# Kernel optimization log

Measured on AMD Instinct MI355X. Metric: run time of the kernel, lower is better.

## Reference

```python
import jax, jax.numpy as jnp
import numpy as np

N_NODES = 100000
NEG_SLOPE = 0.01  # torch F.leaky_relu default

def _degrees(edge_src, edge_dst, n):
    ones = jnp.ones(edge_src.shape[0], dtype=jnp.float32)
    dout = jax.ops.segment_sum(ones, edge_src, num_segments=n)
    din = jax.ops.segment_sum(ones, edge_dst, num_segments=n)
    # DGL clamps zero degrees to 1 (norm='both')
    dout_inv_sqrt = jax.lax.rsqrt(jnp.maximum(dout, 1.0))
    din_inv_sqrt = jax.lax.rsqrt(jnp.maximum(din, 1.0))
    return dout_inv_sqrt, din_inv_sqrt

def _graph_conv(x, W, b, edge_src, edge_dst, dout_is, din_is, n):
    # DGL GraphConv, norm='both': h_i = b + sum_{j->i} (x_j W) / sqrt(d_out(j) d_in(i))
    h = (x * dout_is[:, None]) @ W            # [N, out]
    agg = jax.ops.segment_sum(h[edge_src], edge_dst, num_segments=n)
    return agg * din_is[:, None] + b

def setup_inputs() -> dict:
    key = jax.random.key(0)
    ks = jax.random.split(key, 16)
    n, e = N_NODES, 1600000
    features = jax.random.normal(ks[0], (n, 4), dtype=jnp.float32)
    edge_src = jax.random.randint(ks[1], (e,), 0, n, dtype=jnp.int32)
    edge_dst = jax.random.randint(ks[2], (e,), 0, n, dtype=jnp.int32)
    dims = [(4, 128), (128, 128), (128, 128), (128, 128), (128, 3)]
    inp = {"features": features, "edge_src": edge_src, "edge_dst": edge_dst}
    for i, (fi, fo) in enumerate(dims):
        s = (2.0 / (fi + fo)) ** 0.5  # glorot
        inp[f"W{i+1}"] = jax.random.normal(ks[3 + i], (fi, fo), dtype=jnp.float32) * s
        inp[f"b{i+1}"] = jnp.zeros((fo,), dtype=jnp.float32)
    return inp

def reference(features, edge_src, edge_dst, W1, b1, W2, b2, W3, b3, W4, b4, W5, b5):
    n = features.shape[0]
    dout_is, din_is = _degrees(edge_src, edge_dst, n)
    lrelu = lambda x: jnp.where(x >= 0, x, NEG_SLOPE * x)
    x = lrelu(_graph_conv(features, W1, b1, edge_src, edge_dst, dout_is, din_is, n))
    x = lrelu(_graph_conv(x, W2, b2, edge_src, edge_dst, dout_is, din_is, n))
    x = lrelu(_graph_conv(x, W3, b3, edge_src, edge_dst, dout_is, din_is, n))
    x = lrelu(_graph_conv(x, W4, b4, edge_src, edge_dst, dout_is, din_is, n))
    x = _graph_conv(x, W5, b5, edge_src, edge_dst, dout_is, din_is, n)
    return x
```

## Files before the change

### kernel.cpp

```cpp
#include <hip/hip_runtime.h>
#include <hip/hip_fp16.h>
#include <math.h>


#define LRELU_SLOPE 0.01f
#define XPAD 129
#define MAXBUCK 512


__device__ inline void chunk_range(int E, int nchunks, int cid, int& lo, int& hi) {
    int chunk = (E + nchunks - 1) / nchunks;
    lo = cid * chunk;
    hi = min(E, lo + chunk);
}

__global__ __launch_bounds__(256) void k_part_hist2(const int* __restrict__ src, const int* __restrict__ dst,
                                                    int E, int nbuck,
                                                    unsigned* __restrict__ gHistS, unsigned* __restrict__ gHistD,
                                                    unsigned* __restrict__ blockBaseS, unsigned* __restrict__ blockBaseD) {
    __shared__ unsigned hs[MAXBUCK];
    __shared__ unsigned hd[MAXBUCK];
    for (int i = threadIdx.x; i < nbuck; i += 256) { hs[i] = 0u; hd[i] = 0u; }
    __syncthreads();
    int lo, hi;
    chunk_range(E, gridDim.x, blockIdx.x, lo, hi);
    for (int e = lo + threadIdx.x; e < hi; e += 256) {
        atomicAdd(&hs[src[e] >> 8], 1u);
        atomicAdd(&hd[dst[e] >> 8], 1u);
    }
    __syncthreads();
    for (int i = threadIdx.x; i < nbuck; i += 256) {
        blockBaseS[(size_t)blockIdx.x * nbuck + i] = atomicAdd(&gHistS[i], hs[i]);
        blockBaseD[(size_t)blockIdx.x * nbuck + i] = atomicAdd(&gHistD[i], hd[i]);
    }
}

__global__ __launch_bounds__(512) void k_part_scan(const unsigned* __restrict__ gHist, int nbuck,
                                                   unsigned* __restrict__ bucketStart,
                                                   unsigned* __restrict__ row_ptr_last, unsigned Eval) {
    __shared__ unsigned s[MAXBUCK];
    int t = threadIdx.x;
    s[t] = (t < nbuck) ? gHist[t] : 0u;
    __syncthreads();
    for (int off = 1; off < MAXBUCK; off <<= 1) {
        unsigned v = (t >= off) ? s[t - off] : 0u;
        __syncthreads();
        s[t] += v;
        __syncthreads();
    }
    if (t <= nbuck) bucketStart[t] = (t == 0) ? 0u : s[t - 1];
    if (t == 0 && row_ptr_last) *row_ptr_last = Eval;
}

__global__ __launch_bounds__(256) void k_part_scatter_both(const int* __restrict__ src, const int* __restrict__ dst,
                                                           int E, int nbuck,
                                                           const unsigned* __restrict__ bstartS,
                                                           const unsigned* __restrict__ bstartD,
                                                           const unsigned* __restrict__ blockBaseS,
                                                           const unsigned* __restrict__ blockBaseD,
                                                           int2* __restrict__ pairs, int* __restrict__ srcbuf) {
    __shared__ unsigned curS[MAXBUCK];
    __shared__ unsigned curD[MAXBUCK];
    for (int i = threadIdx.x; i < nbuck; i += 256) {
        curS[i] = bstartS[i] + blockBaseS[(size_t)blockIdx.x * nbuck + i];
        curD[i] = bstartD[i] + blockBaseD[(size_t)blockIdx.x * nbuck + i];
    }
    __syncthreads();
    int lo, hi;
    chunk_range(E, gridDim.x, blockIdx.x, lo, hi);
    for (int e = lo + threadIdx.x; e < hi; e += 256) {
        int s = src[e], d = dst[e];
        unsigned posD = atomicAdd(&curD[d >> 8], 1u);
        pairs[posD] = make_int2(s, d);
        unsigned posS = atomicAdd(&curS[s >> 8], 1u);
        srcbuf[posS] = s;
    }
}

__global__ __launch_bounds__(256) void k_bucket_csr(const int2* __restrict__ pairs,
                                                    const unsigned* __restrict__ bucketStart,
                                                    unsigned* __restrict__ row_ptr,
                                                    unsigned* __restrict__ din_cnt,
                                                    int* __restrict__ csr, int n) {
    __shared__ unsigned hist[256];
    __shared__ unsigned scanw[256];
    __shared__ unsigned cur[256];
    int b = blockIdx.x, t = threadIdx.x;
    unsigned beg = bucketStart[b], end = bucketStart[b + 1];
    hist[t] = 0u;
    __syncthreads();
    for (unsigned e = beg + t; e < end; e += 256)
        atomicAdd(&hist[pairs[e].y & 255], 1u);
    __syncthreads();
    scanw[t] = hist[t];
    __syncthreads();
    for (int off = 1; off < 256; off <<= 1) {
        unsigned u = (t >= off) ? scanw[t - off] : 0u;
        __syncthreads();
        scanw[t] += u;
        __syncthreads();
    }
    unsigned excl = scanw[t] - hist[t];
    int node = (b << 8) + t;
    if (node < n) {
        row_ptr[node] = beg + excl;
        din_cnt[node] = hist[t];
    }
    cur[t] = excl;
    __syncthreads();
    for (unsigned e = beg + t; e < end; e += 256) {
        int2 p = pairs[e];
        unsigned pos = beg + atomicAdd(&cur[p.y & 255], 1u);
        csr[pos] = p.x;
    }
}

__global__ __launch_bounds__(256) void k_bucket_cnt(const int* __restrict__ vals,
                                                    const unsigned* __restrict__ bucketStart,
                                                    unsigned* __restrict__ dout_cnt, int n) {
    __shared__ unsigned hist[256];
    int b = blockIdx.x, t = threadIdx.x;
    unsigned beg = bucketStart[b], end = bucketStart[b + 1];
    hist[t] = 0u;
    __syncthreads();
    for (unsigned e = beg + t; e < end; e += 256)
        atomicAdd(&hist[vals[e] & 255], 1u);
    __syncthreads();
    int node = (b << 8) + t;
    if (node < n) dout_cnt[node] = hist[t];
}

__global__ void k_invsqrt2(const unsigned* __restrict__ c0, float* __restrict__ i0,
                           const unsigned* __restrict__ c1, float* __restrict__ i1, int n) {
    int i = blockIdx.x * blockDim.x + threadIdx.x;
    if (i < n) {
        i0[i] = 1.0f / sqrtf(fmaxf((float)c0[i], 1.0f));
        i1[i] = 1.0f / sqrtf(fmaxf((float)c1[i], 1.0f));
    }
}


__global__ void k_prescale4(const float* __restrict__ x, const float* __restrict__ dout_is,
                            float* __restrict__ pf4, int n) {
    int i = blockIdx.x * blockDim.x + threadIdx.x;
    if (i >= n) return;
    float s = dout_is[i];
    float4 v = *reinterpret_cast<const float4*>(x + (size_t)i * 4);
    float4 o = {v.x * s, v.y * s, v.z * s, v.w * s};
    *reinterpret_cast<float4*>(pf4 + (size_t)i * 4) = o;
}

__global__ void k_gather4(const float* __restrict__ pf4, const int* __restrict__ csr,
                          const unsigned* __restrict__ row_ptr, const float* __restrict__ din_is,
                          const float* __restrict__ dout_is, float* __restrict__ a4, int n) {
    int i = blockIdx.x * blockDim.x + threadIdx.x;
    if (i >= n) return;
    unsigned beg = row_ptr[i], end = row_ptr[i + 1];
    float4 acc = {0.f, 0.f, 0.f, 0.f};
    unsigned e = beg;
    for (; e + 4 <= end; e += 4) {
        int s0 = csr[e], s1 = csr[e + 1], s2 = csr[e + 2], s3 = csr[e + 3];
        float4 v0 = *reinterpret_cast<const float4*>(pf4 + (size_t)s0 * 4);
        float4 v1 = *reinterpret_cast<const float4*>(pf4 + (size_t)s1 * 4);
        float4 v2 = *reinterpret_cast<const float4*>(pf4 + (size_t)s2 * 4);
        float4 v3 = *reinterpret_cast<const float4*>(pf4 + (size_t)s3 * 4);
        acc.x += (v0.x + v1.x) + (v2.x + v3.x);
        acc.y += (v0.y + v1.y) + (v2.y + v3.y);
        acc.z += (v0.z + v1.z) + (v2.z + v3.z);
        acc.w += (v0.w + v1.w) + (v2.w + v3.w);
    }
    for (; e < end; ++e) {
        int s = csr[e];
        float4 v = *reinterpret_cast<const float4*>(pf4 + (size_t)s * 4);
        acc.x += v.x; acc.y += v.y; acc.z += v.z; acc.w += v.w;
    }
    float sc = din_is[i] * dout_is[i];
    float4 o = {acc.x * sc, acc.y * sc, acc.z * sc, acc.w * sc};
    *reinterpret_cast<float4*>(a4 + (size_t)i * 4) = o;
}


__device__ inline void sth16(__half* p, const float* v) {
    __half2 hh[8];
#pragma unroll
    for (int q = 0; q < 8; ++q) hh[q] = __floats2half2_rn(v[2 * q], v[2 * q + 1]);
    const float4* f = reinterpret_cast<const float4*>(&hh[0]);
    *reinterpret_cast<float4*>(p) = f[0];
    *reinterpret_cast<float4*>(p + 8) = f[1];
}

__device__ inline void acc8(float* acc, uint4 u) {
    const __half2* h = reinterpret_cast<const __half2*>(&u);
#pragma unroll
    for (int q = 0; q < 4; ++q) {
        float2 f = __half22float2(h[q]);
        acc[2 * q] += f.x;
        acc[2 * q + 1] += f.y;
    }
}


__device__ inline float4 xp1_cols(float4 av, float ds, float4 wa, float4 wb, float4 wc, float4 wd, float4 bc) {
    float4 r;
    r.x = fmaf(av.x, wa.x, fmaf(av.y, wb.x, fmaf(av.z, wc.x, fmaf(av.w, wd.x, ds * bc.x))));
    r.y = fmaf(av.x, wa.y, fmaf(av.y, wb.y, fmaf(av.z, wc.y, fmaf(av.w, wd.y, ds * bc.y))));
    r.z = fmaf(av.x, wa.z, fmaf(av.y, wb.z, fmaf(av.z, wc.z, fmaf(av.w, wd.z, ds * bc.z))));
    r.w = fmaf(av.x, wa.w, fmaf(av.y, wb.w, fmaf(av.z, wc.w, fmaf(av.w, wd.w, ds * bc.w))));
    r.x = (r.x >= 0.f) ? r.x : LRELU_SLOPE * r.x;
    r.y = (r.y >= 0.f) ? r.y : LRELU_SLOPE * r.y;
    r.z = (r.z >= 0.f) ? r.z : LRELU_SLOPE * r.z;
    r.w = (r.w >= 0.f) ? r.w : LRELU_SLOPE * r.w;
    return r;
}

__global__ __launch_bounds__(512) void k_gl12(const float* __restrict__ a4,
                                              const float* __restrict__ dout_v,
                                              const int* __restrict__ csr,
                                              const unsigned* __restrict__ row_ptr,
                                              const float* __restrict__ din_is, const float* __restrict__ dout_is,
                                              const float* __restrict__ W1, const float* __restrict__ b1,
                                              const float* __restrict__ W2, const float* __restrict__ b2,
                                              __half* __restrict__ xh_out, int n) {
    __shared__ float xs[64 * XPAD];
    const int t = threadIdx.x;
    const int bbase = blockIdx.x * 64;
    const int wave = t >> 6;
    const int lane = t & 63;
    const int half = lane >> 5;
    const int j4 = (lane & 31) * 4;

    float4 wa = *reinterpret_cast<const float4*>(W1 + 0 * 128 + j4);
    float4 wb = *reinterpret_cast<const float4*>(W1 + 1 * 128 + j4);
    float4 wc = *reinterpret_cast<const float4*>(W1 + 2 * 128 + j4);
    float4 wd = *reinterpret_cast<const float4*>(W1 + 3 * 128 + j4);
    float4 bc = *reinterpret_cast<const float4*>(b1 + j4);

#pragma unroll
    for (int sweep = 0; sweep < 4; ++sweep) {
        int r = wave * 2 + half + sweep * 16;
        int node = bbase + r;
        float4 acc = {0.f, 0.f, 0.f, 0.f};
        if (node < n) {
            unsigned beg = row_ptr[node], end = row_ptr[node + 1];
            unsigned e = beg;
            for (; e + 4 <= end; e += 4) {
                int s0 = csr[e + 0], s1 = csr[e + 1], s2 = csr[e + 2], s3 = csr[e + 3];
                float4 a0 = *reinterpret_cast<const float4*>(a4 + (size_t)s0 * 4);
                float4 a1 = *reinterpret_cast<const float4*>(a4 + (size_t)s1 * 4);
                float4 a2 = *reinterpret_cast<const float4*>(a4 + (size_t)s2 * 4);
                float4 a3 = *reinterpret_cast<const float4*>(a4 + (size_t)s3 * 4);
                float d0 = dout_v[s0], d1 = dout_v[s1], d2 = dout_v[s2], d3 = dout_v[s3];
                float4 x0 = xp1_cols(a0, d0, wa, wb, wc, wd, bc);
                float4 x1 = xp1_cols(a1, d1, wa, wb, wc, wd, bc);
                float4 x2 = xp1_cols(a2, d2, wa, wb, wc, wd, bc);
                float4 x3 = xp1_cols(a3, d3, wa, wb, wc, wd, bc);
                acc.x += (x0.x + x1.x) + (x2.x + x3.x);
                acc.y += (x0.y + x1.y) + (x2.y + x3.y);
                acc.z += (x0.z + x1.z) + (x2.z + x3.z);
                acc.w += (x0.w + x1.w) + (x2.w + x3.w);
            }
            for (; e < end; ++e) {
                int s = csr[e];
                float4 av = *reinterpret_cast<const float4*>(a4 + (size_t)s * 4);
                float4 xv = xp1_cols(av, dout_v[s], wa, wb, wc, wd, bc);
                acc.x += xv.x; acc.y += xv.y; acc.z += xv.z; acc.w += xv.w;
            }
            float di = din_is[node];
            acc.x *= di; acc.y *= di; acc.z *= di; acc.w *= di;
        }
        float* d = xs + r * XPAD + j4;
        d[0] = acc.x; d[1] = acc.y; d[2] = acc.z; d[3] = acc.w;
    }
    __syncthreads();

    const int jg = __builtin_amdgcn_readfirstlane(wave) & 7;
    const int j0 = jg * 16;
    const float* Wj = W2 + j0;
    const float* xrow = xs + lane * XPAD;

    float acc[16];
#pragma unroll
    for (int q = 0; q < 16; ++q) acc[q] = 0.f;

#pragma unroll 2
    for (int k = 0; k < 128; k += 4) {
        float x0 = xrow[k + 0];
        float x1 = xrow[k + 1];
        float x2 = xrow[k + 2];
        float x3 = xrow[k + 3];
        const float* w0 = Wj + (size_t)k * 128;
#pragma unroll
        for (int q = 0; q < 16; ++q) {
            acc[q] += x0 * w0[q] + x1 * w0[128 + q] + x2 * w0[256 + q] + x3 * w0[384 + q];
        }
    }

    int node = bbase + lane;
    if (node < n) {
        float s = dout_is[node];
        float v[16];
#pragma unroll
        for (int q = 0; q < 16; ++q) {
            float u = acc[q] + b2[j0 + q];
            u = (u >= 0.f) ? u : LRELU_SLOPE * u;
            v[q] = u * s;
        }
        sth16(xh_out + (size_t)node * 128 + j0, v);
    }
}


#define GATHER_FP16_TILE(XH)                                                         \
    for (int sweep = 0; sweep < 4; ++sweep) {                                        \
        int r = wave * 2 + half + sweep * 16;                                        \
        int node = bbase + r;                                                        \
        float acc[8];                                                                \
        _Pragma("unroll") for (int q = 0; q < 8; ++q) acc[q] = 0.f;                  \
        float di = 0.f;                                                              \
        if (node < n) {                                                              \
            unsigned beg = row_ptr[node], end = row_ptr[node + 1];                   \
            unsigned e = beg;                                                        \
            for (; e + 8 <= end; e += 8) {                                           \
                int s0 = csr[e + 0 + sub];                                           \
                int s1 = csr[e + 2 + sub];                                           \
                int s2 = csr[e + 4 + sub];                                           \
                int s3 = csr[e + 6 + sub];                                           \
                uint4 u0 = *reinterpret_cast<const uint4*>(XH + (size_t)s0 * 128 + c8); \
                uint4 u1 = *reinterpret_cast<const uint4*>(XH + (size_t)s1 * 128 + c8); \
                uint4 u2 = *reinterpret_cast<const uint4*>(XH + (size_t)s2 * 128 + c8); \
                uint4 u3 = *reinterpret_cast<const uint4*>(XH + (size_t)s3 * 128 + c8); \
                acc8(acc, u0); acc8(acc, u1); acc8(acc, u2); acc8(acc, u3);          \
            }                                                                        \
            for (; e + 2 <= end; e += 2) {                                           \
                int s = csr[e + sub];                                                \
                acc8(acc, *reinterpret_cast<const uint4*>(XH + (size_t)s * 128 + c8)); \
            }                                                                        \
            if (e < end && sub == 0) {                                               \
                int s = csr[e];                                                      \
                acc8(acc, *reinterpret_cast<const uint4*>(XH + (size_t)s * 128 + c8)); \
            }                                                                        \
            di = din_is[node];                                                       \
        }                                                                            \
        _Pragma("unroll") for (int q = 0; q < 8; ++q)                                \
            acc[q] += __shfl_xor(acc[q], 16, 64);                                    \
        if (sub == 0) {                                                              \
            float* d = xs + r * XPAD + c8;                                           \
            _Pragma("unroll") for (int q = 0; q < 8; ++q) d[q] = acc[q] * di;        \
        }                                                                            \
    }


__global__ __launch_bounds__(512) void k_gl128h(const __half* __restrict__ xh, const int* __restrict__ csr,
                                                const unsigned* __restrict__ row_ptr,
                                                const float* __restrict__ din_is, const float* __restrict__ dout_is,
                                                const float* __restrict__ W, const float* __restrict__ b,
                                                __half* __restrict__ xh_out, int n) {
    __shared__ float xs[64 * XPAD];
    const int t = threadIdx.x;
    const int bbase = blockIdx.x * 64;
    const int wave = t >> 6;
    const int lane = t & 63;
    const int half = lane >> 5;
    const int sub = (lane >> 4) & 1;
    const int c8 = (lane & 15) * 8;

    GATHER_FP16_TILE(xh)
    __syncthreads();

    const int jg = __builtin_amdgcn_readfirstlane(wave) & 7;
    const int j0 = jg * 16;
    const float* Wj = W + j0;
    const float* xrow = xs + lane * XPAD;

    float acc[16];
#pragma unroll
    for (int q = 0; q < 16; ++q) acc[q] = 0.f;

#pragma unroll 2
    for (int k = 0; k < 128; k += 4) {
        float x0 = xrow[k + 0];
        float x1 = xrow[k + 1];
        float x2 = xrow[k + 2];
        float x3 = xrow[k + 3];
        const float* w0 = Wj + (size_t)k * 128;
#pragma unroll
        for (int q = 0; q < 16; ++q) {
            acc[q] += x0 * w0[q] + x1 * w0[128 + q] + x2 * w0[256 + q] + x3 * w0[384 + q];
        }
    }

    int node = bbase + lane;
    if (node < n) {
        float s = dout_is[node];
        float v[16];
#pragma unroll
        for (int q = 0; q < 16; ++q) {
            float u = acc[q] + b[j0 + q];
            u = (u >= 0.f) ? u : LRELU_SLOPE * u;
            v[q] = u * s;
        }
        sth16(xh_out + (size_t)node * 128 + j0, v);
    }
}


__global__ __launch_bounds__(512) void k_gl128f(const __half* __restrict__ xh, const int* __restrict__ csr,
                                                const unsigned* __restrict__ row_ptr,
                                                const float* __restrict__ din_is, const float* __restrict__ dout_is,
                                                const float* __restrict__ W, const float* __restrict__ b,
                                                const float* __restrict__ W5,
                                                float* __restrict__ h5, int n) {
    __shared__ float xs[64 * XPAD];
    const int t = threadIdx.x;
    const int bbase = blockIdx.x * 64;
    const int wave = t >> 6;
    const int lane = t & 63;
    const int half = lane >> 5;
    const int sub = (lane >> 4) & 1;
    const int c8 = (lane & 15) * 8;

    GATHER_FP16_TILE(xh)
    __syncthreads();

    const int jg = __builtin_amdgcn_readfirstlane(wave) & 7;
    const int j0 = jg * 16;
    const float* Wj = W + j0;
    const float* xrow = xs + lane * XPAD;

    float acc[16];
#pragma unroll
    for (int q = 0; q < 16; ++q) acc[q] = 0.f;

#pragma unroll 2
    for (int k = 0; k < 128; k += 4) {
        float x0 = xrow[k + 0];
        float x1 = xrow[k + 1];
        float x2 = xrow[k + 2];
        float x3 = xrow[k + 3];
        const float* w0 = Wj + (size_t)k * 128;
#pragma unroll
        for (int q = 0; q < 16; ++q) {
            acc[q] += x0 * w0[q] + x1 * w0[128 + q] + x2 * w0[256 + q] + x3 * w0[384 + q];
        }
    }

    float s = (bbase + lane < n) ? dout_is[bbase + lane] : 0.f;
    float p0 = 0.f, p1 = 0.f, p2 = 0.f;
#pragma unroll
    for (int q = 0; q < 16; ++q) {
        float u = acc[q] + b[j0 + q];
        u = (u >= 0.f) ? u : LRELU_SLOPE * u;
        u *= s;
        const float* w5r = W5 + (size_t)(j0 + q) * 3;
        p0 = fmaf(u, w5r[0], p0);
        p1 = fmaf(u, w5r[1], p1);
        p2 = fmaf(u, w5r[2], p2);
    }
    __syncthreads();
    float* red = xs;
    red[lane * 24 + wave * 3 + 0] = p0;
    red[lane * 24 + wave * 3 + 1] = p1;
    red[lane * 24 + wave * 3 + 2] = p2;
    __syncthreads();
    if (t < 64) {
        int node = bbase + t;
        if (node < n) {
            float a0 = 0.f, a1 = 0.f, a2 = 0.f;
#pragma unroll
            for (int w = 0; w < 8; ++w) {
                a0 += red[t * 24 + w * 3 + 0];
                a1 += red[t * 24 + w * 3 + 1];
                a2 += red[t * 24 + w * 3 + 2];
            }
            h5[(size_t)node * 3 + 0] = a0;
            h5[(size_t)node * 3 + 1] = a1;
            h5[(size_t)node * 3 + 2] = a2;
        }
    }
}


__global__ void k_gather3(const float* __restrict__ h, const int* __restrict__ csr,
                          const unsigned* __restrict__ row_ptr, const float* __restrict__ din_is,
                          const float* __restrict__ b, float* __restrict__ out, int n) {
    int i = blockIdx.x * blockDim.x + threadIdx.x;
    if (i >= n) return;
    unsigned beg = row_ptr[i], end = row_ptr[i + 1];
    float a0 = 0.f, a1 = 0.f, a2 = 0.f;
    for (unsigned e = beg; e < end; ++e) {
        int s = csr[e];
        a0 += h[(size_t)s * 3 + 0];
        a1 += h[(size_t)s * 3 + 1];
        a2 += h[(size_t)s * 3 + 2];
    }
    float di = din_is[i];
    out[(size_t)i * 3 + 0] = a0 * di + b[0];
    out[(size_t)i * 3 + 1] = a1 * di + b[1];
    out[(size_t)i * 3 + 2] = a2 * di + b[2];
}


extern "C" void kernel_launch(void* const* d_in, const int* in_sizes, int n_in,
                              void* d_out, int out_size, void* d_ws, size_t ws_size,
                              hipStream_t stream) {
    const float* features = (const float*)d_in[0];
    const int* esrc = (const int*)d_in[1];
    const int* edst = (const int*)d_in[2];
    const float* W1 = (const float*)d_in[3];  const float* b1 = (const float*)d_in[4];
    const float* W2 = (const float*)d_in[5];  const float* b2 = (const float*)d_in[6];
    const float* W3 = (const float*)d_in[7];  const float* b3 = (const float*)d_in[8];
    const float* W4 = (const float*)d_in[9];  const float* b4 = (const float*)d_in[10];
    const float* W5 = (const float*)d_in[11]; const float* b5 = (const float*)d_in[12];

    const int N = in_sizes[0] / 4;
    const int E = in_sizes[1];
    const int nbuck = (N + 255) / 256;
    const int NPB = 256;

    size_t off = 0;
    auto carve = [&](size_t bytes) -> void* {
        void* p = (char*)d_ws + off;
        off = (off + bytes + 255) & ~(size_t)255;
        return p;
    };
    char*     scratch   = (char*)carve((size_t)E * 12 + 256);
    float*    Bp        = (float*)carve((size_t)N * 8 * 4);
    __half*   xh2       = (__half*)carve((size_t)N * 128 * 2);
    __half*   xh3       = (__half*)carve((size_t)N * 128 * 2);
    int*      csr       = (int*)carve((size_t)E * 4);
    unsigned* row_ptr   = (unsigned*)carve((size_t)(N + 1) * 4);
    unsigned* dout_cnt  = (unsigned*)carve((size_t)N * 4);
    unsigned* din_cnt   = (unsigned*)carve((size_t)N * 4);
    float*    dout_is   = (float*)carve((size_t)N * 4);
    float*    din_is    = (float*)carve((size_t)N * 4);
    unsigned* gHistD    = (unsigned*)carve((size_t)MAXBUCK * 4);
    unsigned* gHistS    = (unsigned*)carve((size_t)MAXBUCK * 4);
    unsigned* bstartD   = (unsigned*)carve((size_t)(MAXBUCK + 1) * 4);
    unsigned* bstartS   = (unsigned*)carve((size_t)(MAXBUCK + 1) * 4);
    unsigned* blockBaseD = (unsigned*)carve((size_t)NPB * nbuck * 4);
    unsigned* blockBaseS = (unsigned*)carve((size_t)NPB * nbuck * 4);
    float*    h5        = (float*)carve((size_t)N * 3 * 4);
    (void)ws_size;
    int2* pairs  = (int2*)scratch;
    int*  srcbuf = (int*)(scratch + (size_t)E * 8);
    float* pf4 = Bp;
    float* a4  = Bp + (size_t)N * 4;

    hipMemsetAsync(gHistD, 0, (size_t)MAXBUCK * 4, stream);
    hipMemsetAsync(gHistS, 0, (size_t)MAXBUCK * 4, stream);

    k_part_hist2<<<NPB, 256, 0, stream>>>(esrc, edst, E, nbuck, gHistS, gHistD, blockBaseS, blockBaseD);
    k_part_scan<<<1, 512, 0, stream>>>(gHistD, nbuck, bstartD, row_ptr + N, (unsigned)E);
    k_part_scan<<<1, 512, 0, stream>>>(gHistS, nbuck, bstartS, (unsigned*)nullptr, 0u);
    k_part_scatter_both<<<NPB, 256, 0, stream>>>(esrc, edst, E, nbuck, bstartS, bstartD,
                                                 blockBaseS, blockBaseD, pairs, srcbuf);
    k_bucket_csr<<<nbuck, 256, 0, stream>>>(pairs, bstartD, row_ptr, din_cnt, csr, N);
    k_bucket_cnt<<<nbuck, 256, 0, stream>>>(srcbuf, bstartS, dout_cnt, N);
    k_invsqrt2<<<(N + 255) / 256, 256, 0, stream>>>(dout_cnt, dout_is, din_cnt, din_is, N);

    k_prescale4<<<(N + 255) / 256, 256, 0, stream>>>(features, dout_is, pf4, N);
    k_gather4<<<(N + 255) / 256, 256, 0, stream>>>(pf4, csr, row_ptr, din_is, dout_is, a4, N);

    int glGrid = (N + 63) / 64;
    k_gl12<<<glGrid, 512, 0, stream>>>(a4, dout_is, csr, row_ptr, din_is, dout_is, W1, b1, W2, b2, xh2, N);
    k_gl128h<<<glGrid, 512, 0, stream>>>(xh2, csr, row_ptr, din_is, dout_is, W3, b3, xh3, N);
    k_gl128f<<<glGrid, 512, 0, stream>>>(xh3, csr, row_ptr, din_is, dout_is, W4, b4, W5, h5, N);

    k_gather3<<<(N + 255) / 256, 256, 0, stream>>>(h5, csr, row_ptr, din_is, b5, (float*)d_out, N);
}
```

Baseline: 437.3 us.

## Degree-sort rows within each tile to balance gather work across waves

Adds a per-tile bitonic sort of the 64 nodes by in-degree using wave shuffles. Each gather sweep then processes nodes in degree-rank order, so the rows a wave or half-wave handles together have similar edge counts and less lane divergence. The layer-1 gather is restructured to one node per wave with two columns per lane, scalar edge indices via readfirstlane, and a serpentine rank assignment across waves. Leaky ReLU becomes fmaxf. The sort adds shuffle overhead, and the single-node-per-wave layer-1 loop gives up the previous 4-edge unroll.

Result: slower. 491.9 us (+12.5%).

```diff
diff --git a/kernel.cpp b/kernel.cpp
--- a/kernel.cpp
+++ b/kernel.cpp
@@ -199,19 +199,26 @@
     }
 }
 
-
-__device__ inline float4 xp1_cols(float4 av, float ds, float4 wa, float4 wb, float4 wc, float4 wd, float4 bc) {
-    float4 r;
-    r.x = fmaf(av.x, wa.x, fmaf(av.y, wb.x, fmaf(av.z, wc.x, fmaf(av.w, wd.x, ds * bc.x))));
-    r.y = fmaf(av.x, wa.y, fmaf(av.y, wb.y, fmaf(av.z, wc.y, fmaf(av.w, wd.y, ds * bc.y))));
-    r.z = fmaf(av.x, wa.z, fmaf(av.y, wb.z, fmaf(av.z, wc.z, fmaf(av.w, wd.z, ds * bc.z))));
-    r.w = fmaf(av.x, wa.w, fmaf(av.y, wb.w, fmaf(av.z, wc.w, fmaf(av.w, wd.w, ds * bc.w))));
-    r.x = (r.x >= 0.f) ? r.x : LRELU_SLOPE * r.x;
-    r.y = (r.y >= 0.f) ? r.y : LRELU_SLOPE * r.y;
-    r.z = (r.z >= 0.f) ? r.z : LRELU_SLOPE * r.z;
-    r.w = (r.w >= 0.f) ? r.w : LRELU_SLOPE * r.w;
-    return r;
-}
+__device__ inline int degree_rank_row(const unsigned* __restrict__ row_ptr,
+                                      int bbase, int lane, int n) {
+    int node0 = bbase + lane;
+    int deg = 0;
+    if (node0 < n) deg = (int)(row_ptr[node0 + 1] - row_ptr[node0]);
+    int key = (deg << 8) | lane;
+#pragma unroll
+    for (int k = 2; k <= 64; k <<= 1) {
+#pragma unroll
+        for (int j = k >> 1; j >= 1; j >>= 1) {
+            int other = __shfl_xor(key, j, 64);
+            bool up = ((lane & k) == 0);
+            bool lower = ((lane & j) == 0);
+            int mn = min(key, other), mx = max(key, other);
+            key = (up == lower) ? mn : mx;
+        }
+    }
+    return key & 255;
+}
+
 
 __global__ __launch_bounds__(512) void k_gl12(const float* __restrict__ a4,
                                               const float* __restrict__ dout_v,
@@ -224,57 +231,48 @@
     __shared__ float xs[64 * XPAD];
     const int t = threadIdx.x;
     const int bbase = blockIdx.x * 64;
-    const int wave = t >> 6;
+    const int wave = __builtin_amdgcn_readfirstlane(t >> 6) & 7;
     const int lane = t & 63;
-    const int half = lane >> 5;
-    const int j4 = (lane & 31) * 4;
-
-    float4 wa = *reinterpret_cast<const float4*>(W1 + 0 * 128 + j4);
-    float4 wb = *reinterpret_cast<const float4*>(W1 + 1 * 128 + j4);
-    float4 wc = *reinterpret_cast<const float4*>(W1 + 2 * 128 + j4);
-    float4 wd = *reinterpret_cast<const float4*>(W1 + 3 * 128 + j4);
-    float4 bc = *reinterpret_cast<const float4*>(b1 + j4);
-
-#pragma unroll
-    for (int sweep = 0; sweep < 4; ++sweep) {
-        int r = wave * 2 + half + sweep * 16;
+    const int j2 = lane * 2;
+
+    float2 w10 = make_float2(W1[0 * 128 + j2], W1[0 * 128 + j2 + 1]);
+    float2 w11 = make_float2(W1[1 * 128 + j2], W1[1 * 128 + j2 + 1]);
+    float2 w12 = make_float2(W1[2 * 128 + j2], W1[2 * 128 + j2 + 1]);
+    float2 w13 = make_float2(W1[3 * 128 + j2], W1[3 * 128 + j2 + 1]);
+    float2 bc2 = make_float2(b1[j2], b1[j2 + 1]);
+
+    const int Lr = degree_rank_row(row_ptr, bbase, lane, n);
+
+    for (int sweep = 0; sweep < 8; ++sweep) {
+        int rank = sweep * 8 + ((sweep & 1) ? (7 - wave) : wave);
+        int r = __builtin_amdgcn_readfirstlane(__shfl(Lr, rank, 64));
         int node = bbase + r;
-        float4 acc = {0.f, 0.f, 0.f, 0.f};
+        float accx = 0.f, accy = 0.f;
+        float di = 0.f;
         if (node < n) {
-            unsigned beg = row_ptr[node], end = row_ptr[node + 1];
-            unsigned e = beg;
-            for (; e + 4 <= end; e += 4) {
-                int s0 = csr[e + 0], s1 = csr[e + 1], s2 = csr[e + 2], s3 = csr[e + 3];
-                float4 a0 = *reinterpret_cast<const float4*>(a4 + (size_t)s0 * 4);
-                float4 a1 = *reinterpret_cast<const float4*>(a4 + (size_t)s1 * 4);
-                float4 a2 = *reinterpret_cast<const float4*>(a4 + (size_t)s2 * 4);
-                float4 a3 = *reinterpret_cast<const float4*>(a4 + (size_t)s3 * 4);
-                float d0 = dout_v[s0], d1 = dout_v[s1], d2 = dout_v[s2], d3 = dout_v[s3];
-                float4 x0 = xp1_cols(a0, d0, wa, wb, wc, wd, bc);
-                float4 x1 = xp1_cols(a1, d1, wa, wb, wc, wd, bc);
-                float4 x2 = xp1_cols(a2, d2, wa, wb, wc, wd, bc);
-                float4 x3 = xp1_cols(a3, d3, wa, wb, wc, wd, bc);
-                acc.x += (x0.x + x1.x) + (x2.x + x3.x);
-                acc.y += (x0.y + x1.y) + (x2.y + x3.y);
-                acc.z += (x0.z + x1.z) + (x2.z + x3.z);
-                acc.w += (x0.w + x1.w) + (x2.w + x3.w);
+            unsigned beg = __builtin_amdgcn_readfirstlane(row_ptr[node]);
+            unsigned end = __builtin_amdgcn_readfirstlane(row_ptr[node + 1]);
+#pragma unroll 2
+            for (unsigned e = beg; e < end; ++e) {
+                int s = __builtin_amdgcn_readfirstlane(csr[e]);
+                float4 av = *reinterpret_cast<const float4*>(a4 + (size_t)s * 4);
+                float ds = dout_v[s];
+                float y0 = fmaf(av.x, w10.x, fmaf(av.y, w11.x, fmaf(av.z, w12.x, fmaf(av.w, w13.x, ds * bc2.x))));
+                float y1 = fmaf(av.x, w10.y, fmaf(av.y, w11.y, fmaf(av.z, w12.y, fmaf(av.w, w13.y, ds * bc2.y))));
+                y0 = fmaxf(y0, LRELU_SLOPE * y0);
+                y1 = fmaxf(y1, LRELU_SLOPE * y1);
+                accx += y0;
+                accy += y1;
             }
-            for (; e < end; ++e) {
-                int s = csr[e];
-                float4 av = *reinterpret_cast<const float4*>(a4 + (size_t)s * 4);
-                float4 xv = xp1_cols(av, dout_v[s], wa, wb, wc, wd, bc);
-                acc.x += xv.x; acc.y += xv.y; acc.z += xv.z; acc.w += xv.w;
-            }
-            float di = din_is[node];
-            acc.x *= di; acc.y *= di; acc.z *= di; acc.w *= di;
-        }
-        float* d = xs + r * XPAD + j4;
-        d[0] = acc.x; d[1] = acc.y; d[2] = acc.z; d[3] = acc.w;
-    }
-    __syncthreads();
-
-    const int jg = __builtin_amdgcn_readfirstlane(wave) & 7;
-    const int j0 = jg * 16;
+            di = din_is[node];
+        }
+        float* d = xs + r * XPAD + j2;
+        d[0] = accx * di;
+        d[1] = accy * di;
+    }
+    __syncthreads();
+
+    const int j0 = wave * 16;
     const float* Wj = W2 + j0;
     const float* xrow = xs + lane * XPAD;
 
@@ -302,7 +300,7 @@
 #pragma unroll
         for (int q = 0; q < 16; ++q) {
             float u = acc[q] + b2[j0 + q];
-            u = (u >= 0.f) ? u : LRELU_SLOPE * u;
+            u = fmaxf(u, LRELU_SLOPE * u);
             v[q] = u * s;
         }
         sth16(xh_out + (size_t)node * 128 + j0, v);
@@ -312,7 +310,8 @@
 
 #define GATHER_FP16_TILE(XH)                                                         \
     for (int sweep = 0; sweep < 4; ++sweep) {                                        \
-        int r = wave * 2 + half + sweep * 16;                                        \
+        int rank = wave * 2 + half + sweep * 16;                                     \
+        int r = __shfl(Lr, rank, 64);                                                \
         int node = bbase + r;                                                        \
         float acc[8];                                                                \
         _Pragma("unroll") for (int q = 0; q < 8; ++q) acc[q] = 0.f;                  \
@@ -364,6 +363,8 @@
     const int sub = (lane >> 4) & 1;
     const int c8 = (lane & 15) * 8;
 
+    const int Lr = degree_rank_row(row_ptr, bbase, lane, n);
+
     GATHER_FP16_TILE(xh)
     __syncthreads();
 
@@ -396,7 +397,7 @@
 #pragma unroll
         for (int q = 0; q < 16; ++q) {
             float u = acc[q] + b[j0 + q];
-            u = (u >= 0.f) ? u : LRELU_SLOPE * u;
+            u = fmaxf(u, LRELU_SLOPE * u);
             v[q] = u * s;
         }
         sth16(xh_out + (size_t)node * 128 + j0, v);
@@ -419,6 +420,8 @@
     const int sub = (lane >> 4) & 1;
     const int c8 = (lane & 15) * 8;
 
+    const int Lr = degree_rank_row(row_ptr, bbase, lane, n);
+
     GATHER_FP16_TILE(xh)
     __syncthreads();
 
@@ -449,7 +452,7 @@
 #pragma unroll
     for (int q = 0; q < 16; ++q) {
         float u = acc[q] + b[j0 + q];
-        u = (u >= 0.f) ? u : LRELU_SLOPE * u;
+        u = fmaxf(u, LRELU_SLOPE * u);
         u *= s;
         const float* w5r = W5 + (size_t)(j0 + q) * 3;
         p0 = fmaf(u, w5r[0], p0);
```
